# Kernel optimization log

Hardware: AMD Instinct MI355X
Metric: run time of the kernel (lower is better)

The kernel has to match this reference:

```python
import jax, jax.numpy as jnp
import numpy as np

NUM_SEQS = 8
SEQ_LEN = 2048
HIDDEN = 768
NUM_HEADS = 12
HEAD_DIM = 64
EPS = 1e-12


def setup_inputs() -> dict:
    key = jax.random.key(0)
    ks = jax.random.split(key, 12)
    total = NUM_SEQS * SEQ_LEN
    hidden_states = jax.random.normal(ks[0], (total, HIDDEN), dtype=jnp.float32)
    cu_seq_lens = jnp.arange(NUM_SEQS + 1, dtype=jnp.int32) * SEQ_LEN
    s = 0.02
    inp = {
        "hidden_states": hidden_states,
        "cu_seq_lens": cu_seq_lens,
        "max_seq_len": SEQ_LEN,
        "norm_w": jnp.ones((HIDDEN,), jnp.float32),
        "norm_b": jnp.zeros((HIDDEN,), jnp.float32),
        "Wq": jax.random.normal(ks[1], (HIDDEN, HIDDEN), jnp.float32) * s,
        "bq": jnp.zeros((HIDDEN,), jnp.float32),
        "Wk": jax.random.normal(ks[2], (HIDDEN, HIDDEN), jnp.float32) * s,
        "bk": jnp.zeros((HIDDEN,), jnp.float32),
        "Wv": jax.random.normal(ks[3], (HIDDEN, HIDDEN), jnp.float32) * s,
        "bv": jnp.zeros((HIDDEN,), jnp.float32),
        "Wo": jax.random.normal(ks[4], (HIDDEN, HIDDEN), jnp.float32) * s,
        "bo": jnp.zeros((HIDDEN,), jnp.float32),
    }
    return inp


def _layer_norm(x, w, b):
    mu = jnp.mean(x, axis=-1, keepdims=True)
    var = jnp.mean(jnp.square(x - mu), axis=-1, keepdims=True)
    return (x - mu) * jax.lax.rsqrt(var + EPS) * w + b


def _rope(x, positions, interleaved=False):
    # x: [t, h, d]; positions: [t]
    d = x.shape[-1]
    inv_freq = 1.0 / (10000.0 ** (jnp.arange(0, d, 2, dtype=jnp.float32) / d))  # [d/2]
    theta = positions.astype(jnp.float32)[:, None] * inv_freq[None, :]  # [t, d/2]
    cos = jnp.cos(theta)[:, None, :]  # [t, 1, d/2]
    sin = jnp.sin(theta)[:, None, :]
    x1, x2 = x[..., : d // 2], x[..., d // 2 :]
    return jnp.concatenate([x1 * cos - x2 * sin, x2 * cos + x1 * sin], axis=-1)


def _attention(q, k, v):
    # q,k,v: [b, s, h, d] (equal-length sequences, no padding)
    scale = 1.0 / jnp.sqrt(jnp.asarray(q.shape[-1], q.dtype))
    scores = jnp.einsum("bqhd,bkhd->bhqk", q, k) * scale
    probs = jax.nn.softmax(scores, axis=-1)
    return jnp.einsum("bhqk,bkhd->bqhd", probs, v)


def reference(hidden_states, cu_seq_lens, max_seq_len, norm_w, norm_b,
              Wq, bq, Wk, bk, Wv, bv, Wo, bo):
    t = hidden_states.shape[0]
    # pre_norm, layer_idx=1 -> LayerNorm
    x = _layer_norm(hidden_states, norm_w, norm_b)
    value = x @ Wv + bv
    query = x @ Wq + bq
    key = x @ Wk + bk

    def split(z):
        return z.reshape(t, NUM_HEADS, HEAD_DIM)

    q, k, v = split(query), split(key), split(value)

    # positions within each sequence (equal-length packing)
    positions = jnp.tile(jnp.arange(SEQ_LEN, dtype=jnp.int32), NUM_SEQS)
    q = _rope(q, positions)
    k = _rope(k, positions)

    # reshape packed -> [b, s, h, d]; sequences are equal-length here
    qb = q.reshape(NUM_SEQS, SEQ_LEN, NUM_HEADS, HEAD_DIM)
    kb = k.reshape(NUM_SEQS, SEQ_LEN, NUM_HEADS, HEAD_DIM)
    vb = v.reshape(NUM_SEQS, SEQ_LEN, NUM_HEADS, HEAD_DIM)
    attn = _attention(qb, kb, vb).reshape(t, HIDDEN)

    attn = attn @ Wo + bo
    # residual add (dropout prob = 0)
    out = attn + x
    return out
```

## Files before the change

### kernel.cpp

```cpp
#include <hip/hip_runtime.h>

typedef __bf16 bf16x8 __attribute__((ext_vector_type(8)));
typedef float  f32x4  __attribute__((ext_vector_type(4)));
typedef float  f32x16 __attribute__((ext_vector_type(16)));
typedef unsigned u32x2 __attribute__((ext_vector_type(2)));

#define MFMA16(a,b,c) __builtin_amdgcn_mfma_f32_16x16x32_bf16((a),(b),(c),0,0,0)
#define MFMA32(a,b,c) __builtin_amdgcn_mfma_f32_32x32x16_bf16((a),(b),(c),0,0,0)

constexpr int  HID  = 768;
constexpr long T    = 16384;
constexpr long SZ   = T * HID;
constexpr int  SEQ  = 2048;
constexpr int  NH   = 12;
constexpr int  HD   = 64;
constexpr int  WELE = HID * HID;

constexpr float QSCALE = 0.125f * 1.4426950408889634f;
constexpr float L10K32 = 13.287712379549449f / 32.0f;

__device__ __forceinline__ unsigned pkbf(float a, float b) {
    union { __bf16 h[2]; unsigned u; } x;
    x.h[0] = (__bf16)a; x.h[1] = (__bf16)b; return x.u;
}

__device__ __forceinline__ void gld16(const __bf16* g, __bf16* l) {
    __builtin_amdgcn_global_load_lds(
        (const __attribute__((address_space(1))) unsigned int*)g,
        (__attribute__((address_space(3))) unsigned int*)l, 16, 0, 0);
}

__global__ __launch_bounds__(256)
void wconv_kernel(const float* __restrict__ W0, __bf16* __restrict__ T0,
                  const float* __restrict__ W1, __bf16* __restrict__ T1,
                  const float* __restrict__ W2, __bf16* __restrict__ T2,
                  const float* __restrict__ W3, __bf16* __restrict__ T3) {
    const float* W; __bf16* Wt;
    switch (blockIdx.z) {
        case 0: W = W0; Wt = T0; break;
        case 1: W = W1; Wt = T1; break;
        case 2: W = W2; Wt = T2; break;
        default: W = W3; Wt = T3; break;
    }
    __shared__ float tile[64][65];
    int n0 = blockIdx.x * 64, k0 = blockIdx.y * 64;
    int c = threadIdx.x & 63, rr = threadIdx.x >> 6;
#pragma unroll
    for (int i = 0; i < 16; i++) {
        int r = i * 4 + rr;
        tile[r][c] = W[(long)(k0 + r) * HID + n0 + c];
    }
    __syncthreads();
#pragma unroll
    for (int i = 0; i < 16; i++) {
        int r = i * 4 + rr;
        Wt[(long)(n0 + r) * HID + k0 + c] = (__bf16)tile[c][r];
    }
}

__global__ __launch_bounds__(256)
void ln_kernel(const float* __restrict__ hs, const float* __restrict__ w,
               const float* __restrict__ b, __bf16* __restrict__ xbf) {
    int row = blockIdx.x, tid = threadIdx.x;
    const float* hr = hs + (long)row * HID;
    float v0 = hr[tid], v1 = hr[tid + 256], v2 = hr[tid + 512];
    float s  = v0 + v1 + v2;
    float s2 = v0 * v0 + v1 * v1 + v2 * v2;
#pragma unroll
    for (int off = 1; off < 64; off <<= 1) {
        s  += __shfl_xor(s, off);
        s2 += __shfl_xor(s2, off);
    }
    __shared__ float red[8];
    int wave = tid >> 6;
    if ((tid & 63) == 0) { red[wave] = s; red[4 + wave] = s2; }
    __syncthreads();
    s  = red[0] + red[1] + red[2] + red[3];
    s2 = red[4] + red[5] + red[6] + red[7];
    float mu   = s * (1.0f / HID);
    float var  = s2 * (1.0f / HID) - mu * mu;
    float rstd = rsqrtf(var + 1e-12f);
    long base = (long)row * HID;
    xbf[base + tid]       = (__bf16)((v0 - mu) * rstd * w[tid]       + b[tid]);
    xbf[base + tid + 256] = (__bf16)((v1 - mu) * rstd * w[tid + 256] + b[tid + 256]);
    xbf[base + tid + 512] = (__bf16)((v2 - mu) * rstd * w[tid + 512] + b[tid + 512]);
}

constexpr int SEGSZ = 528;

template <int MODE>
__global__ __launch_bounds__(256)
void gemm_lds(const __bf16* __restrict__ A, const __bf16* __restrict__ Bt,
              const float* __restrict__ bias, __bf16* __restrict__ outb,
              const __bf16* __restrict__ resid, float* __restrict__ outf,
              float scale) {
    int tid = threadIdx.x, wave = tid >> 6, lane = tid & 63;
    int lr = lane & 15, quad = lane >> 4;
    int wm = wave >> 1, wn = wave & 1;
    long m0 = (long)blockIdx.x * 128;
    int  n0 = blockIdx.y * 128;

    __shared__ __align__(16) __bf16 As[16 * SEGSZ];
    __shared__ __align__(16) __bf16 Bs[16 * SEGSZ];

    const f32x4 vzero = {0.f, 0.f, 0.f, 0.f};
    f32x4 acc[4][4];
#pragma unroll
    for (int ms = 0; ms < 4; ms++)
#pragma unroll
        for (int ns = 0; ns < 4; ns++) acc[ms][ns] = vzero;

    const __bf16* ga = A  + (long)(m0 + wave * 32 + (lane >> 3)) * HID + (lane & 7) * 8;
    const __bf16* gb = Bt + (long)(n0 + wave * 32 + (lane >> 3)) * HID + (lane & 7) * 8;
    __bf16* la = As + wave * 4 * SEGSZ;
    __bf16* lb = Bs + wave * 4 * SEGSZ;

    int fbase = (lr >> 3) * SEGSZ + (lr & 7) * 64 + quad * 8;

    for (int k0 = 0; k0 < HID; k0 += 64) {
#pragma unroll
        for (int j = 0; j < 4; j++) {
            gld16(ga + (long)j * 8 * HID + k0, la + j * SEGSZ);
            gld16(gb + (long)j * 8 * HID + k0, lb + j * SEGSZ);
        }
        __syncthreads();
#pragma unroll
        for (int kk = 0; kk < 64; kk += 32) {
            bf16x8 af[4], bfr[4];
#pragma unroll
            for (int ms = 0; ms < 4; ms++)
                af[ms] = *(const bf16x8*)&As[fbase + (wm * 8 + ms * 2) * SEGSZ + kk];
#pragma unroll
            for (int ns = 0; ns < 4; ns++)
                bfr[ns] = *(const bf16x8*)&Bs[fbase + (wn * 8 + ns * 2) * SEGSZ + kk];
#pragma unroll
            for (int ms = 0; ms < 4; ms++)
#pragma unroll
                for (int ns = 0; ns < 4; ns++)
                    acc[ms][ns] = MFMA16(af[ms], bfr[ns], acc[ms][ns]);
        }
        __syncthreads();
    }

    if (MODE == 3) {
        int hb = n0 + wn * 64;
        float f1 = __builtin_amdgcn_exp2f(-(float)lr * L10K32);
        float f2 = __builtin_amdgcn_exp2f(-(float)(lr + 16) * L10K32);
        float b0 = bias[hb + lr],      b1 = bias[hb + 16 + lr];
        float b2 = bias[hb + 32 + lr], b3 = bias[hb + 48 + lr];
#pragma unroll
        for (int ms = 0; ms < 4; ms++)
#pragma unroll
        for (int r = 0; r < 4; r++) {
            long row = m0 + wm * 64 + ms * 16 + quad * 4 + r;
            int pos = (int)(row & (SEQ - 1));
            float s1, c1, s2, c2;
            __sincosf((float)pos * f1, &s1, &c1);
            __sincosf((float)pos * f2, &s2, &c2);
            float v0 = acc[ms][0][r] + b0, v1 = acc[ms][1][r] + b1;
            float v2 = acc[ms][2][r] + b2, v3 = acc[ms][3][r] + b3;
            __bf16* ob = outb + row * HID + hb;
            ob[lr]      = (__bf16)((v0 * c1 - v2 * s1) * scale);
            ob[16 + lr] = (__bf16)((v1 * c2 - v3 * s2) * scale);
            ob[32 + lr] = (__bf16)((v2 * c1 + v0 * s1) * scale);
            ob[48 + lr] = (__bf16)((v3 * c2 + v1 * s2) * scale);
        }
    } else if (MODE == 1) {
#pragma unroll
        for (int ms = 0; ms < 4; ms++)
#pragma unroll
        for (int r = 0; r < 4; r++) {
            int d = (int)(m0 + wm * 64 + ms * 16 + quad * 4 + r);
            float bv = bias[d];
            int hh = d >> 6, dd = d & 63;
#pragma unroll
            for (int ns = 0; ns < 4; ns++) {
                int posg = n0 + wn * 64 + ns * 16 + lr;
                int sq = posg >> 11, pos = posg & (SEQ - 1);
                outb[((long)((sq * NH + hh) * HD + dd) << 11) + pos] =
                    (__bf16)(acc[ms][ns][r] + bv);
            }
        }
    } else {
#pragma unroll
        for (int ns = 0; ns < 4; ns++) {
            int col = n0 + wn * 64 + ns * 16 + lr;
            float bv = bias[col];
#pragma unroll
            for (int ms = 0; ms < 4; ms++)
#pragma unroll
            for (int r = 0; r < 4; r++) {
                long row = m0 + wm * 64 + ms * 16 + quad * 4 + r;
                outf[row * HID + col] = acc[ms][ns][r] + bv + (float)resid[row * HID + col];
            }
        }
    }
}

__global__ __launch_bounds__(256)
void attn_kernel(const __bf16* __restrict__ q, const __bf16* __restrict__ k,
                 const __bf16* __restrict__ vt, __bf16* __restrict__ att) {
    int tid = threadIdx.x, wave = tid >> 6, lane = tid & 63;
    int c = lane & 31, hi = lane >> 5;
    int bb = blockIdx.x;
    int s  = bb & 7;
    int ii = bb >> 3;
    int h  = ii >> 4;
    int qt = ii & 15;
    long q0 = (long)s * SEQ + qt * 128 + wave * 32;

    __shared__ __align__(16) __bf16 Ks[2][64 * 64];
    __shared__ __align__(16) __bf16 Vs[2][64 * 64];

    bf16x8 qf[4];
    {
        const __bf16* qrow = q + (q0 + c) * HID + h * HD + hi * 8;
#pragma unroll
        for (int kk = 0; kk < 4; kk++)
            qf[kk] = *(const bf16x8*)(qrow + kk * 16);
    }

    f32x16 o[2] = {};
    float ls = 0.f;

    const __bf16* kg = k  + (long)s * SEQ * HID + h * HD;
    const __bf16* vg = vt + (long)(s * NH + h) * HD * SEQ;

    int srow = lane >> 3;
    int sgch = (lane & 7) ^ srow;

#define STAGE(bufi, kv)                                                         \
    {                                                                           \
        _Pragma("unroll")                                                       \
        for (int rr = 0; rr < 2; rr++) {                                        \
            int grp = rr * 4 + wave;                                            \
            gld16(kg + (long)((kv) + grp * 8 + srow) * HID + sgch * 8,          \
                  &Ks[bufi][grp * 8 * 64]);                                     \
            gld16(vg + (long)(grp * 8 + srow) * SEQ + (kv) + sgch * 8,          \
                  &Vs[bufi][grp * 8 * 64]);                                     \
        }                                                                       \
    }

    STAGE(0, 0)
    __syncthreads();

    for (int kt = 0; kt < SEQ / 64; kt++) {
        int cur = kt & 1;
        if (kt < SEQ / 64 - 1) STAGE(cur ^ 1, (kt + 1) * 64)

        f32x16 st[2];
        __builtin_amdgcn_s_setprio(1);
#pragma unroll
        for (int kh = 0; kh < 2; kh++) {
            f32x16 acc = {};
            int R = kh * 32 + c;
#pragma unroll
            for (int kk = 0; kk < 4; kk++) {
                bf16x8 kf = *(const bf16x8*)
                    &Ks[cur][R * 64 + ((((kk << 1) + hi) ^ (R & 7)) << 3)];
                acc = MFMA32(kf, qf[kk], acc);
            }
            st[kh] = acc;
        }
        __builtin_amdgcn_s_setprio(0);

        float s0 = 0.f, s1 = 0.f;
#pragma unroll
        for (int r = 0; r < 16; r++) {
            float e0 = __builtin_amdgcn_exp2f(st[0][r]);
            float e1 = __builtin_amdgcn_exp2f(st[1][r]);
            st[0][r] = e0; s0 += e0;
            st[1][r] = e1; s1 += e1;
        }
        ls += s0 + s1;

        bf16x8 pb[4];
#pragma unroll
        for (int kh = 0; kh < 2; kh++) {
            unsigned pk[8];
#pragma unroll
            for (int i = 0; i < 8; i++)
                pk[i] = pkbf(st[kh][2 * i], st[kh][2 * i + 1]);
#pragma unroll
            for (int b = 0; b < 2; b++) {
                u32x2 r02 = __builtin_amdgcn_permlane32_swap(
                    pk[4 * b + 0], pk[4 * b + 2], false, false);
                u32x2 r13 = __builtin_amdgcn_permlane32_swap(
                    pk[4 * b + 1], pk[4 * b + 3], false, false);
                union { unsigned u[4]; bf16x8 v; } pu;
                pu.u[0] = r02[0]; pu.u[1] = r13[0];
                pu.u[2] = r02[1]; pu.u[3] = r13[1];
                pb[2 * kh + b] = pu.v;
            }
        }

        __builtin_amdgcn_s_setprio(1);
#pragma unroll
        for (int dh = 0; dh < 2; dh++) {
            int R = dh * 32 + c;
#pragma unroll
            for (int kk = 0; kk < 4; kk++) {
                bf16x8 vf = *(const bf16x8*)
                    &Vs[cur][R * 64 + ((((kk << 1) + hi) ^ (R & 7)) << 3)];
                o[dh] = MFMA32(vf, pb[kk], o[dh]);
            }
        }
        __builtin_amdgcn_s_setprio(0);

        __syncthreads();
    }
#undef STAGE

    ls += __shfl_xor(ls, 32);
    float inv = 1.0f / ls;
    __bf16* ob = att + (q0 + c) * HID + h * HD;
#pragma unroll
    for (int dh = 0; dh < 2; dh++)
#pragma unroll
        for (int a = 0; a < 4; a++) {
            unsigned lo  = pkbf(o[dh][4 * a] * inv,     o[dh][4 * a + 1] * inv);
            unsigned hi2 = pkbf(o[dh][4 * a + 2] * inv, o[dh][4 * a + 3] * inv);
            int d = dh * 32 + a * 8 + hi * 4;
            *(unsigned long long*)&ob[d] =
                ((unsigned long long)hi2 << 32) | lo;
        }
}

extern "C" void kernel_launch(void* const* d_in, const int* in_sizes, int n_in,
                              void* d_out, int out_size, void* d_ws, size_t ws_size,
                              hipStream_t stream) {
    const float* hs    = (const float*)d_in[0];
    const float* normw = (const float*)d_in[3];
    const float* normb = (const float*)d_in[4];
    const float* Wq = (const float*)d_in[5];
    const float* bq = (const float*)d_in[6];
    const float* Wk = (const float*)d_in[7];
    const float* bk = (const float*)d_in[8];
    const float* Wv = (const float*)d_in[9];
    const float* bv = (const float*)d_in[10];
    const float* Wo = (const float*)d_in[11];
    const float* bo = (const float*)d_in[12];

    __bf16* base = (__bf16*)d_ws;
    __bf16* x   = base;
    __bf16* qb  = base + SZ;
    __bf16* kb  = base + 2 * SZ;
    __bf16* vtb = base + 3 * SZ;
    __bf16* att = base + 4 * SZ;
    __bf16* wqt = base + 5 * SZ;
    __bf16* wkt = wqt + WELE;
    __bf16* wvt = wkt + WELE;
    __bf16* wot = wvt + WELE;

    wconv_kernel<<<dim3(12, 12, 4), 256, 0, stream>>>(Wq, wqt, Wk, wkt, Wv, wvt, Wo, wot);

    ln_kernel<<<(int)T, 256, 0, stream>>>(hs, normw, normb, x);

    gemm_lds<3><<<dim3(T / 128, HID / 128), 256, 0, stream>>>(x, wqt, bq, qb, nullptr, nullptr, QSCALE);
    gemm_lds<3><<<dim3(T / 128, HID / 128), 256, 0, stream>>>(x, wkt, bk, kb, nullptr, nullptr, 1.0f);
    gemm_lds<1><<<dim3(HID / 128, T / 128), 256, 0, stream>>>(wvt, x, bv, vtb, nullptr, nullptr, 1.0f);

    attn_kernel<<<dim3(NH * 16 * 8), 256, 0, stream>>>(qb, kb, vtb, att);

    gemm_lds<2><<<dim3(T / 128, HID / 128), 256, 0, stream>>>(att, wot, bo, nullptr, x, (float*)d_out, 1.0f);
}
```

Measured before the change: 411.8 us.

## Fuse Q/K projection GEMMs and compute softmax row sums via MFMA in attention

Result: faster. 398.8 us (-3.2%).

```diff
diff --git a/kernel.cpp b/kernel.cpp
--- a/kernel.cpp
+++ b/kernel.cpp
@@ -142,12 +142,105 @@
         __syncthreads();
     }
 
-    if (MODE == 3) {
-        int hb = n0 + wn * 64;
-        float f1 = __builtin_amdgcn_exp2f(-(float)lr * L10K32);
-        float f2 = __builtin_amdgcn_exp2f(-(float)(lr + 16) * L10K32);
-        float b0 = bias[hb + lr],      b1 = bias[hb + 16 + lr];
-        float b2 = bias[hb + 32 + lr], b3 = bias[hb + 48 + lr];
+    if (MODE == 1) {
+#pragma unroll
+        for (int ms = 0; ms < 4; ms++)
+#pragma unroll
+        for (int r = 0; r < 4; r++) {
+            int d = (int)(m0 + wm * 64 + ms * 16 + quad * 4 + r);
+            float bv = bias[d];
+            int hh = d >> 6, dd = d & 63;
+#pragma unroll
+            for (int ns = 0; ns < 4; ns++) {
+                int posg = n0 + wn * 64 + ns * 16 + lr;
+                int sq = posg >> 11, pos = posg & (SEQ - 1);
+                outb[((long)((sq * NH + hh) * HD + dd) << 11) + pos] =
+                    (__bf16)(acc[ms][ns][r] + bv);
+            }
+        }
+    } else {
+#pragma unroll
+        for (int ns = 0; ns < 4; ns++) {
+            int col = n0 + wn * 64 + ns * 16 + lr;
+            float bv = bias[col];
+#pragma unroll
+            for (int ms = 0; ms < 4; ms++)
+#pragma unroll
+            for (int r = 0; r < 4; r++) {
+                long row = m0 + wm * 64 + ms * 16 + quad * 4 + r;
+                outf[row * HID + col] = acc[ms][ns][r] + bv + (float)resid[row * HID + col];
+            }
+        }
+    }
+}
+
+__global__ __launch_bounds__(256, 2)
+void gemm_qk(const __bf16* __restrict__ A, const __bf16* __restrict__ Btq,
+             const __bf16* __restrict__ Btk,
+             const float* __restrict__ biasq, const float* __restrict__ biask,
+             __bf16* __restrict__ outq, __bf16* __restrict__ outk) {
+    int tid = threadIdx.x, wave = tid >> 6, lane = tid & 63;
+    int lr = lane & 15, quad = lane >> 4;
+    int wm = wave >> 1, wn = wave & 1;
+    long m0 = (long)blockIdx.x * 128;
+    int  n0 = blockIdx.y * 128;
+
+    __shared__ __align__(16) __bf16 As[16 * SEGSZ];
+    __shared__ __align__(16) __bf16 Bqs[16 * SEGSZ];
+    __shared__ __align__(16) __bf16 Bks[16 * SEGSZ];
+
+    const f32x4 vzero = {0.f, 0.f, 0.f, 0.f};
+    f32x4 accq[4][4], acck[4][4];
+#pragma unroll
+    for (int ms = 0; ms < 4; ms++)
+#pragma unroll
+        for (int ns = 0; ns < 4; ns++) { accq[ms][ns] = vzero; acck[ms][ns] = vzero; }
+
+    const __bf16* ga = A   + (long)(m0 + wave * 32 + (lane >> 3)) * HID + (lane & 7) * 8;
+    const __bf16* gq = Btq + (long)(n0 + wave * 32 + (lane >> 3)) * HID + (lane & 7) * 8;
+    const __bf16* gk = Btk + (long)(n0 + wave * 32 + (lane >> 3)) * HID + (lane & 7) * 8;
+    __bf16* la = As  + wave * 4 * SEGSZ;
+    __bf16* lq = Bqs + wave * 4 * SEGSZ;
+    __bf16* lk = Bks + wave * 4 * SEGSZ;
+
+    int fbase = (lr >> 3) * SEGSZ + (lr & 7) * 64 + quad * 8;
+
+    for (int k0 = 0; k0 < HID; k0 += 64) {
+#pragma unroll
+        for (int j = 0; j < 4; j++) {
+            gld16(ga + (long)j * 8 * HID + k0, la + j * SEGSZ);
+            gld16(gq + (long)j * 8 * HID + k0, lq + j * SEGSZ);
+            gld16(gk + (long)j * 8 * HID + k0, lk + j * SEGSZ);
+        }
+        __syncthreads();
+#pragma unroll
+        for (int kk = 0; kk < 64; kk += 32) {
+            bf16x8 af[4], bqf[4], bkf[4];
+#pragma unroll
+            for (int ms = 0; ms < 4; ms++)
+                af[ms] = *(const bf16x8*)&As[fbase + (wm * 8 + ms * 2) * SEGSZ + kk];
+#pragma unroll
+            for (int ns = 0; ns < 4; ns++) {
+                bqf[ns] = *(const bf16x8*)&Bqs[fbase + (wn * 8 + ns * 2) * SEGSZ + kk];
+                bkf[ns] = *(const bf16x8*)&Bks[fbase + (wn * 8 + ns * 2) * SEGSZ + kk];
+            }
+#pragma unroll
+            for (int ms = 0; ms < 4; ms++)
+#pragma unroll
+                for (int ns = 0; ns < 4; ns++) {
+                    accq[ms][ns] = MFMA16(af[ms], bqf[ns], accq[ms][ns]);
+                    acck[ms][ns] = MFMA16(af[ms], bkf[ns], acck[ms][ns]);
+                }
+        }
+        __syncthreads();
+    }
+
+    int hb = n0 + wn * 64;
+    float f1 = __builtin_amdgcn_exp2f(-(float)lr * L10K32);
+    float f2 = __builtin_amdgcn_exp2f(-(float)(lr + 16) * L10K32);
+    {
+        float b0 = biasq[hb + lr],      b1 = biasq[hb + 16 + lr];
+        float b2 = biasq[hb + 32 + lr], b3 = biasq[hb + 48 + lr];
 #pragma unroll
         for (int ms = 0; ms < 4; ms++)
 #pragma unroll
@@ -157,42 +250,34 @@
             float s1, c1, s2, c2;
             __sincosf((float)pos * f1, &s1, &c1);
             __sincosf((float)pos * f2, &s2, &c2);
-            float v0 = acc[ms][0][r] + b0, v1 = acc[ms][1][r] + b1;
-            float v2 = acc[ms][2][r] + b2, v3 = acc[ms][3][r] + b3;
-            __bf16* ob = outb + row * HID + hb;
-            ob[lr]      = (__bf16)((v0 * c1 - v2 * s1) * scale);
-            ob[16 + lr] = (__bf16)((v1 * c2 - v3 * s2) * scale);
-            ob[32 + lr] = (__bf16)((v2 * c1 + v0 * s1) * scale);
-            ob[48 + lr] = (__bf16)((v3 * c2 + v1 * s2) * scale);
-        }
-    } else if (MODE == 1) {
+            float v0 = accq[ms][0][r] + b0, v1 = accq[ms][1][r] + b1;
+            float v2 = accq[ms][2][r] + b2, v3 = accq[ms][3][r] + b3;
+            __bf16* ob = outq + row * HID + hb;
+            ob[lr]      = (__bf16)((v0 * c1 - v2 * s1) * QSCALE);
+            ob[16 + lr] = (__bf16)((v1 * c2 - v3 * s2) * QSCALE);
+            ob[32 + lr] = (__bf16)((v2 * c1 + v0 * s1) * QSCALE);
+            ob[48 + lr] = (__bf16)((v3 * c2 + v1 * s2) * QSCALE);
+        }
+    }
+    {
+        float b0 = biask[hb + lr],      b1 = biask[hb + 16 + lr];
+        float b2 = biask[hb + 32 + lr], b3 = biask[hb + 48 + lr];
 #pragma unroll
         for (int ms = 0; ms < 4; ms++)
 #pragma unroll
         for (int r = 0; r < 4; r++) {
-            int d = (int)(m0 + wm * 64 + ms * 16 + quad * 4 + r);
-            float bv = bias[d];
-            int hh = d >> 6, dd = d & 63;
-#pragma unroll
-            for (int ns = 0; ns < 4; ns++) {
-                int posg = n0 + wn * 64 + ns * 16 + lr;
-                int sq = posg >> 11, pos = posg & (SEQ - 1);
-                outb[((long)((sq * NH + hh) * HD + dd) << 11) + pos] =
-                    (__bf16)(acc[ms][ns][r] + bv);
-            }
-        }
-    } else {
-#pragma unroll
-        for (int ns = 0; ns < 4; ns++) {
-            int col = n0 + wn * 64 + ns * 16 + lr;
-            float bv = bias[col];
-#pragma unroll
-            for (int ms = 0; ms < 4; ms++)
-#pragma unroll
-            for (int r = 0; r < 4; r++) {
-                long row = m0 + wm * 64 + ms * 16 + quad * 4 + r;
-                outf[row * HID + col] = acc[ms][ns][r] + bv + (float)resid[row * HID + col];
-            }
+            long row = m0 + wm * 64 + ms * 16 + quad * 4 + r;
+            int pos = (int)(row & (SEQ - 1));
+            float s1, c1, s2, c2;
+            __sincosf((float)pos * f1, &s1, &c1);
+            __sincosf((float)pos * f2, &s2, &c2);
+            float v0 = acck[ms][0][r] + b0, v1 = acck[ms][1][r] + b1;
+            float v2 = acck[ms][2][r] + b2, v3 = acck[ms][3][r] + b3;
+            __bf16* ob = outk + row * HID + hb;
+            ob[lr]      = (__bf16)(v0 * c1 - v2 * s1);
+            ob[16 + lr] = (__bf16)(v1 * c2 - v3 * s2);
+            ob[32 + lr] = (__bf16)(v2 * c1 + v0 * s1);
+            ob[48 + lr] = (__bf16)(v3 * c2 + v1 * s2);
         }
     }
 }
@@ -220,8 +305,11 @@
             qf[kk] = *(const bf16x8*)(qrow + kk * 16);
     }
 
+    const __bf16 onebf = (__bf16)1.0f;
+    const bf16x8 ones = {onebf, onebf, onebf, onebf, onebf, onebf, onebf, onebf};
+
     f32x16 o[2] = {};
-    float ls = 0.f;
+    f32x16 lsx = {};
 
     const __bf16* kg = k  + (long)s * SEQ * HID + h * HD;
     const __bf16* vg = vt + (long)(s * NH + h) * HD * SEQ;
@@ -241,78 +329,72 @@
         }                                                                       \
     }
 
+#define ATTN_BODY(BUF)                                                          \
+    {                                                                           \
+        f32x16 st0 = {}, st1 = {};                                              \
+        __builtin_amdgcn_s_setprio(1);                                          \
+        _Pragma("unroll")                                                       \
+        for (int kk = 0; kk < 4; kk++) {                                        \
+            bf16x8 kf0 = *(const bf16x8*)                                       \
+                &Ks[BUF][c * 64 + ((((kk << 1) + hi) ^ (c & 7)) << 3)];         \
+            st0 = MFMA32(kf0, qf[kk], st0);                                     \
+            bf16x8 kf1 = *(const bf16x8*)                                       \
+                &Ks[BUF][(32 + c) * 64 + ((((kk << 1) + hi) ^ (c & 7)) << 3)];  \
+            st1 = MFMA32(kf1, qf[kk], st1);                                     \
+        }                                                                       \
+        __builtin_amdgcn_s_setprio(0);                                          \
+        bf16x8 pb[4];                                                           \
+        _Pragma("unroll")                                                       \
+        for (int kh = 0; kh < 2; kh++) {                                        \
+            unsigned pk[8];                                                     \
+            _Pragma("unroll")                                                   \
+            for (int i = 0; i < 8; i++) {                                       \
+                float e0 = __builtin_amdgcn_exp2f(kh ? st1[2 * i] : st0[2 * i]);        \
+                float e1 = __builtin_amdgcn_exp2f(kh ? st1[2 * i + 1] : st0[2 * i + 1]);\
+                pk[i] = pkbf(e0, e1);                                           \
+            }                                                                   \
+            _Pragma("unroll")                                                   \
+            for (int b = 0; b < 2; b++) {                                       \
+                u32x2 r02 = __builtin_amdgcn_permlane32_swap(                   \
+                    pk[4 * b + 0], pk[4 * b + 2], false, false);                \
+                u32x2 r13 = __builtin_amdgcn_permlane32_swap(                   \
+                    pk[4 * b + 1], pk[4 * b + 3], false, false);                \
+                union { unsigned u[4]; bf16x8 v; } pu;                          \
+                pu.u[0] = r02[0]; pu.u[1] = r13[0];                             \
+                pu.u[2] = r02[1]; pu.u[3] = r13[1];                             \
+                pb[2 * kh + b] = pu.v;                                          \
+            }                                                                   \
+        }                                                                       \
+        __builtin_amdgcn_s_setprio(1);                                          \
+        _Pragma("unroll")                                                       \
+        for (int kk = 0; kk < 4; kk++) {                                        \
+            lsx = MFMA32(ones, pb[kk], lsx);                                    \
+            bf16x8 vf0 = *(const bf16x8*)                                       \
+                &Vs[BUF][c * 64 + ((((kk << 1) + hi) ^ (c & 7)) << 3)];         \
+            o[0] = MFMA32(vf0, pb[kk], o[0]);                                   \
+            bf16x8 vf1 = *(const bf16x8*)                                       \
+                &Vs[BUF][(32 + c) * 64 + ((((kk << 1) + hi) ^ (c & 7)) << 3)];  \
+            o[1] = MFMA32(vf1, pb[kk], o[1]);                                   \
+        }                                                                       \
+        __builtin_amdgcn_s_setprio(0);                                          \
+    }
+
     STAGE(0, 0)
     __syncthreads();
 
-    for (int kt = 0; kt < SEQ / 64; kt++) {
-        int cur = kt & 1;
-        if (kt < SEQ / 64 - 1) STAGE(cur ^ 1, (kt + 1) * 64)
-
-        f32x16 st[2];
-        __builtin_amdgcn_s_setprio(1);
-#pragma unroll
-        for (int kh = 0; kh < 2; kh++) {
-            f32x16 acc = {};
-            int R = kh * 32 + c;
-#pragma unroll
-            for (int kk = 0; kk < 4; kk++) {
-                bf16x8 kf = *(const bf16x8*)
-                    &Ks[cur][R * 64 + ((((kk << 1) + hi) ^ (R & 7)) << 3)];
-                acc = MFMA32(kf, qf[kk], acc);
-            }
-            st[kh] = acc;
-        }
-        __builtin_amdgcn_s_setprio(0);
-
-        float s0 = 0.f, s1 = 0.f;
-#pragma unroll
-        for (int r = 0; r < 16; r++) {
-            float e0 = __builtin_amdgcn_exp2f(st[0][r]);
-            float e1 = __builtin_amdgcn_exp2f(st[1][r]);
-            st[0][r] = e0; s0 += e0;
-            st[1][r] = e1; s1 += e1;
-        }
-        ls += s0 + s1;
-
-        bf16x8 pb[4];
-#pragma unroll
-        for (int kh = 0; kh < 2; kh++) {
-            unsigned pk[8];
-#pragma unroll
-            for (int i = 0; i < 8; i++)
-                pk[i] = pkbf(st[kh][2 * i], st[kh][2 * i + 1]);
-#pragma unroll
-            for (int b = 0; b < 2; b++) {
-                u32x2 r02 = __builtin_amdgcn_permlane32_swap(
-                    pk[4 * b + 0], pk[4 * b + 2], false, false);
-                u32x2 r13 = __builtin_amdgcn_permlane32_swap(
-                    pk[4 * b + 1], pk[4 * b + 3], false, false);
-                union { unsigned u[4]; bf16x8 v; } pu;
-                pu.u[0] = r02[0]; pu.u[1] = r13[0];
-                pu.u[2] = r02[1]; pu.u[3] = r13[1];
-                pb[2 * kh + b] = pu.v;
-            }
-        }
-
-        __builtin_amdgcn_s_setprio(1);
-#pragma unroll
-        for (int dh = 0; dh < 2; dh++) {
-            int R = dh * 32 + c;
-#pragma unroll
-            for (int kk = 0; kk < 4; kk++) {
-                bf16x8 vf = *(const bf16x8*)
-                    &Vs[cur][R * 64 + ((((kk << 1) + hi) ^ (R & 7)) << 3)];
-                o[dh] = MFMA32(vf, pb[kk], o[dh]);
-            }
-        }
-        __builtin_amdgcn_s_setprio(0);
-
+#pragma unroll 1
+    for (int kt2 = 0; kt2 < 16; kt2++) {
+        STAGE(1, (2 * kt2 + 1) * 64)
+        ATTN_BODY(0)
+        __syncthreads();
+        if (kt2 < 15) STAGE(0, (2 * kt2 + 2) * 64)
+        ATTN_BODY(1)
         __syncthreads();
     }
 #undef STAGE
-
-    ls += __shfl_xor(ls, 32);
-    float inv = 1.0f / ls;
+#undef ATTN_BODY
+
+    float inv = 1.0f / lsx[0];
     __bf16* ob = att + (q0 + c) * HID + h * HD;
 #pragma unroll
     for (int dh = 0; dh < 2; dh++)
@@ -356,8 +438,7 @@
 
     ln_kernel<<<(int)T, 256, 0, stream>>>(hs, normw, normb, x);
 
-    gemm_lds<3><<<dim3(T / 128, HID / 128), 256, 0, stream>>>(x, wqt, bq, qb, nullptr, nullptr, QSCALE);
-    gemm_lds<3><<<dim3(T / 128, HID / 128), 256, 0, stream>>>(x, wkt, bk, kb, nullptr, nullptr, 1.0f);
+    gemm_qk<<<dim3(T / 128, HID / 128), 256, 0, stream>>>(x, wqt, wkt, bq, bk, qb, kb);
     gemm_lds<1><<<dim3(HID / 128, T / 128), 256, 0, stream>>>(wvt, x, bv, vtb, nullptr, nullptr, 1.0f);
 
     attn_kernel<<<dim3(NH * 16 * 8), 256, 0, stream>>>(qb, kb, vtb, att);
```
